# Performance work log

Hardware: AMD Instinct MI355X
Metric: run time of the kernel (lower is better)

The kernel has to match this reference:

```python
import jax, jax.numpy as jnp
import numpy as np

EPS = 1e-6

def poincare_pairwise_distance(x, c):
    """x: (B,N,E) points in Poincare ball, c: (C,E) centroids. Returns (B,N,C)."""
    x2 = jnp.sum(x * x, axis=-1)                  # (B,N)
    c2 = jnp.sum(c * c, axis=-1)                  # (C,)
    xc = jnp.einsum('bne,ce->bnc', x, c)          # (B,N,C)
    sq = jnp.maximum(x2[..., None] + c2[None, None, :] - 2.0 * xc, 0.0)  # ||x-c||^2
    den = (1.0 - x2)[..., None] * (1.0 - c2)[None, None, :]
    arg = 1.0 + 2.0 * sq / jnp.maximum(den, EPS)
    return jnp.arccosh(jnp.maximum(arg, 1.0 + EPS))

def setup_inputs() -> dict:
    key = jax.random.key(0)
    k1, k2 = jax.random.split(key)
    B, N, E, C = 32, 4096, 64, 256
    # scale so points lie strictly inside the unit ball (valid hyperbolic coords)
    node_repr = jax.random.normal(k1, (B, N, E), dtype=jnp.float32) * 0.05
    mask = jnp.ones((B, N, 1), dtype=jnp.float32)
    centroid = jax.random.normal(k2, (C, E), dtype=jnp.float32) * 0.01
    return {"node_repr": node_repr, "mask": mask, "centroid": centroid}

def reference(node_repr, mask, centroid):
    dist = poincare_pairwise_distance(node_repr, centroid)   # (B,N,C)
    dist = dist * mask                                       # mask: (B,N,1) broadcasts
    graph_dist = jnp.sum(dist, axis=1) / jnp.sum(mask, axis=1)  # (B,C)
    return graph_dist, dist
```

## Files before the change

### kernel.cpp

```cpp
#include <hip/hip_runtime.h>
#include <math.h>

#define E_DIM 64
#define C_DIM 256
#define EPS_F 1e-6f
#define LN2_F 0.69314718056f
#define TP    68

typedef __attribute__((ext_vector_type(8))) short short8;
typedef __attribute__((ext_vector_type(4))) float f32x4;

__device__ __forceinline__ unsigned short f2bf(float f) {
    unsigned int u = __float_as_uint(f);
    u += 0x7FFFu + ((u >> 16) & 1u);
    return (unsigned short)(u >> 16);
}

__device__ __forceinline__ short8 pack8(float4 a, float4 b) {
    short8 h;
    h[0] = (short)f2bf(a.x); h[1] = (short)f2bf(a.y);
    h[2] = (short)f2bf(a.z); h[3] = (short)f2bf(a.w);
    h[4] = (short)f2bf(b.x); h[5] = (short)f2bf(b.y);
    h[6] = (short)f2bf(b.z); h[7] = (short)f2bf(b.w);
    return h;
}

#define WS_F    0
#define WS_C2   32768
#define WS_RD2  33792
#define WS_INVM 34816

__global__ __launch_bounds__(C_DIM) void cdist_pre(
    const float* __restrict__ cent,
    const float* __restrict__ mask,
    unsigned char* __restrict__ ws,
    int N)
{
    const int t = threadIdx.x;
    if (blockIdx.x == 0) {
        float r[E_DIM];
        const float* cr = cent + t * E_DIM;
        #pragma unroll
        for (int e = 0; e < E_DIM; e += 4) {
            float4 v = *reinterpret_cast<const float4*>(cr + e);
            r[e] = v.x; r[e+1] = v.y; r[e+2] = v.z; r[e+3] = v.w;
        }
        float c2 = 0.f;
        #pragma unroll
        for (int e = 0; e < E_DIM; ++e) c2 = fmaf(r[e], r[e], c2);
        ((float*)(ws + WS_C2))[t]  = c2;
        ((float*)(ws + WS_RD2))[t] = 2.f / (1.f - c2);

        const int ct16 = t >> 4, l15 = t & 15;
        short8* F = (short8*)(ws + WS_F);
        #pragma unroll
        for (int kf = 0; kf < 2; ++kf) {
            #pragma unroll
            for (int q = 0; q < 4; ++q) {
                short8 h;
                #pragma unroll
                for (int j = 0; j < 8; ++j)
                    h[j] = (short)f2bf(r[kf * 32 + q * 8 + j]);
                F[(ct16 * 2 + kf) * 64 + 16 * q + l15] = h;
            }
        }
    } else {
        const int b = blockIdx.x - 1;
        float s = 0.f;
        for (int n = t; n < N; n += C_DIM) s += mask[(size_t)b * N + n];
        #pragma unroll
        for (int off = 32; off > 0; off >>= 1) s += __shfl_down(s, off, 64);
        __shared__ float partial[4];
        if ((t & 63) == 0) partial[t >> 6] = s;
        __syncthreads();
        if (t == 0) {
            float tot = partial[0] + partial[1] + partial[2] + partial[3];
            ((float*)(ws + WS_INVM))[b] = 1.f / tot;
        }
    }
}

template<int NT_TILES>
__global__ __launch_bounds__(256, 4) void cdist_mfma(
    const float* __restrict__ x,
    const float* __restrict__ mask,
    const unsigned char* __restrict__ ws,
    float*       __restrict__ graph_acc,
    float*       __restrict__ dist,
    int N)
{
    const int tid  = threadIdx.x;
    const int w    = tid >> 6;
    const int lane = tid & 63;
    const int l15  = lane & 15;
    const int q    = lane >> 4;
    const int n0   = blockIdx.x * (NT_TILES * 16);
    const int b    = blockIdx.y;

    __shared__ __align__(16) float sT[4][16 * TP];

    const short8* F    = (const short8*)(ws + WS_F);
    const float*  c2w  = (const float*)(ws + WS_C2);
    const float*  rd2w = (const float*)(ws + WS_RD2);

    short8 bfrag[4][2];
    #pragma unroll
    for (int ct = 0; ct < 4; ++ct)
        #pragma unroll
        for (int kf = 0; kf < 2; ++kf)
            bfrag[ct][kf] = F[((w * 4 + ct) * 2 + kf) * 64 + lane];

    float c2v[4], rd2v[4], gsum[4];
    #pragma unroll
    for (int ct = 0; ct < 4; ++ct) {
        const int c = w * 64 + ct * 16 + l15;
        c2v[ct] = c2w[c]; rd2v[ct] = rd2w[c]; gsum[ct] = 0.f;
    }

    const size_t rowbase = (size_t)b * N + n0;
    float* sW = sT[w];

    const float* xr0 = x + (rowbase + l15) * E_DIM + q * 8;
    float4 v0 = *reinterpret_cast<const float4*>(xr0);
    float4 v1 = *reinterpret_cast<const float4*>(xr0 + 4);
    float4 v2 = *reinterpret_cast<const float4*>(xr0 + 32);
    float4 v3 = *reinterpret_cast<const float4*>(xr0 + 36);
    float  mk = mask[rowbase + l15];

    #pragma unroll 1
    for (int rt = 0; rt < NT_TILES; ++rt) {
        float4 u0 = v0, u1 = v1, u2 = v2, u3 = v3;
        float  mkc = mk;

        if (rt < NT_TILES - 1) {
            const float* xr = x + (rowbase + (rt + 1) * 16 + l15) * E_DIM + q * 8;
            v0 = *reinterpret_cast<const float4*>(xr);
            v1 = *reinterpret_cast<const float4*>(xr + 4);
            v2 = *reinterpret_cast<const float4*>(xr + 32);
            v3 = *reinterpret_cast<const float4*>(xr + 36);
            mk = mask[rowbase + (rt + 1) * 16 + l15];
        }

        float ss = 0.f;
        ss = fmaf(u0.x, u0.x, ss); ss = fmaf(u0.y, u0.y, ss);
        ss = fmaf(u0.z, u0.z, ss); ss = fmaf(u0.w, u0.w, ss);
        ss = fmaf(u1.x, u1.x, ss); ss = fmaf(u1.y, u1.y, ss);
        ss = fmaf(u1.z, u1.z, ss); ss = fmaf(u1.w, u1.w, ss);
        ss = fmaf(u2.x, u2.x, ss); ss = fmaf(u2.y, u2.y, ss);
        ss = fmaf(u2.z, u2.z, ss); ss = fmaf(u2.w, u2.w, ss);
        ss = fmaf(u3.x, u3.x, ss); ss = fmaf(u3.y, u3.y, ss);
        ss = fmaf(u3.z, u3.z, ss); ss = fmaf(u3.w, u3.w, ss);
        ss += __shfl_xor(ss, 16);
        ss += __shfl_xor(ss, 32);

        const float rbrow = __builtin_amdgcn_rcpf(1.f - ss);
        const float krow  = LN2_F * mkc;

        short8 a0 = pack8(u0, u1);
        short8 a1 = pack8(u2, u3);

        f32x4 acc[4];
        #pragma unroll
        for (int ct = 0; ct < 4; ++ct) {
            f32x4 z = {0.f, 0.f, 0.f, 0.f};
            z = __builtin_amdgcn_mfma_f32_16x16x32_bf16(a0, bfrag[ct][0], z, 0, 0, 0);
            z = __builtin_amdgcn_mfma_f32_16x16x32_bf16(a1, bfrag[ct][1], z, 0, 0, 0);
            acc[ct] = z;
        }

        float ar[4], rbr[4], kr[4];
        #pragma unroll
        for (int reg = 0; reg < 4; ++reg) {
            const int src = q * 4 + reg;
            ar[reg]  = __shfl(ss,    src);
            rbr[reg] = __shfl(rbrow, src);
            kr[reg]  = __shfl(krow,  src);
        }

        #pragma unroll
        for (int ct = 0; ct < 4; ++ct) {
            #pragma unroll
            for (int reg = 0; reg < 4; ++reg) {
                const float dot = acc[ct][reg];
                float sq = fmaf(-2.f, dot, ar[reg] + c2v[ct]);
                sq = fmaxf(sq, 0.f);
                float uu = fmaxf(sq * (rbr[reg] * rd2v[ct]), EPS_F);
                float t  = uu + __builtin_amdgcn_sqrtf(fmaf(uu, uu, uu + uu));
                const float d = __builtin_amdgcn_logf(1.f + t) * kr[reg];
                sW[(q * 4 + reg) * TP + ct * 16 + l15] = d;
                gsum[ct] += d;
            }
        }

        #pragma unroll
        for (int i = 0; i < 4; ++i) {
            const int row2 = i * 4 + (lane >> 4);
            const int col2 = (lane & 15) * 4;
            f32x4 val = *reinterpret_cast<const f32x4*>(&sW[row2 * TP + col2]);
            __builtin_nontemporal_store(val, reinterpret_cast<f32x4*>(
                dist + (rowbase + rt * 16 + row2) * C_DIM + w * 64 + col2));
        }
    }

    const float inv = ((const float*)(ws + WS_INVM))[b];
    #pragma unroll
    for (int ct = 0; ct < 4; ++ct) {
        float s = gsum[ct];
        s += __shfl_xor(s, 16);
        s += __shfl_xor(s, 32);
        if (q == 0)
            atomicAdd(&graph_acc[b * C_DIM + w * 64 + ct * 16 + l15], s * inv);
    }
}

extern "C" void kernel_launch(void* const* d_in, const int* in_sizes, int n_in,
                              void* d_out, int out_size, void* d_ws, size_t ws_size,
                              hipStream_t stream) {
    const float* x    = (const float*)d_in[0];
    const float* mask = (const float*)d_in[1];
    const float* cent = (const float*)d_in[2];
    float* out = (float*)d_out;

    const long long BN = in_sizes[1];
    const int E = in_sizes[0] / (int)BN;
    const int C = in_sizes[2] / E;
    const int B = (int)(((long long)out_size - BN * C) / C);
    const int N = (int)(BN / B);

    float* graph_acc = out;
    float* dist_out  = out + (size_t)B * C;
    unsigned char* ws = (unsigned char*)d_ws;

    hipMemsetAsync(graph_acc, 0, (size_t)B * C * sizeof(float), stream);

    cdist_pre<<<dim3(B + 1), C_DIM, 0, stream>>>(cent, mask, ws, N);

    if (N % 128 == 0) {
        cdist_mfma<8><<<dim3(N / 128, B), 256, 0, stream>>>(
            x, mask, ws, graph_acc, dist_out, N);
    } else {
        cdist_mfma<4><<<dim3(N / 64, B), 256, 0, stream>>>(
            x, mask, ws, graph_acc, dist_out, N);
    }
}
```

Measured before the change: 184.4 us.

## Deepen x prefetch to two tiles and fold graph_acc zeroing into pre-kernel

The input prefetch in the main MFMA kernel now holds two tiles in a double-buffered register array and issues each load two iterations ahead, with the loop unrolled by two. This gives global loads more time to land before they are consumed. Separately, the hipMemsetAsync launch is removed and the mask-sum blocks of the pre-kernel zero graph_acc instead, saving one launch. The deeper prefetch raises register pressure, which may hurt occupancy under the 4-waves launch bound.

```diff
diff --git a/kernel.cpp b/kernel.cpp
--- a/kernel.cpp
+++ b/kernel.cpp
@@ -34,6 +34,7 @@
     const float* __restrict__ cent,
     const float* __restrict__ mask,
     unsigned char* __restrict__ ws,
+    float* __restrict__ graph_acc,
     int N)
 {
     const int t = threadIdx.x;
@@ -66,6 +67,7 @@
         }
     } else {
         const int b = blockIdx.x - 1;
+        graph_acc[b * C_DIM + t] = 0.f;
         float s = 0.f;
         for (int n = t; n < N; n += C_DIM) s += mask[(size_t)b * N + n];
         #pragma unroll
@@ -120,26 +122,28 @@
     const size_t rowbase = (size_t)b * N + n0;
     float* sW = sT[w];
 
-    const float* xr0 = x + (rowbase + l15) * E_DIM + q * 8;
-    float4 v0 = *reinterpret_cast<const float4*>(xr0);
-    float4 v1 = *reinterpret_cast<const float4*>(xr0 + 4);
-    float4 v2 = *reinterpret_cast<const float4*>(xr0 + 32);
-    float4 v3 = *reinterpret_cast<const float4*>(xr0 + 36);
-    float  mk = mask[rowbase + l15];
-
-    #pragma unroll 1
+    float4 pv0[2], pv1[2], pv2[2], pv3[2];
+    float  pmk[2];
+    {
+        const float* xr0 = x + (rowbase + l15) * E_DIM + q * 8;
+        pv0[0] = *reinterpret_cast<const float4*>(xr0);
+        pv1[0] = *reinterpret_cast<const float4*>(xr0 + 4);
+        pv2[0] = *reinterpret_cast<const float4*>(xr0 + 32);
+        pv3[0] = *reinterpret_cast<const float4*>(xr0 + 36);
+        pmk[0] = mask[rowbase + l15];
+        const float* xr1 = xr0 + 16 * E_DIM;
+        pv0[1] = *reinterpret_cast<const float4*>(xr1);
+        pv1[1] = *reinterpret_cast<const float4*>(xr1 + 4);
+        pv2[1] = *reinterpret_cast<const float4*>(xr1 + 32);
+        pv3[1] = *reinterpret_cast<const float4*>(xr1 + 36);
+        pmk[1] = mask[rowbase + 16 + l15];
+    }
+
+    #pragma unroll 2
     for (int rt = 0; rt < NT_TILES; ++rt) {
-        float4 u0 = v0, u1 = v1, u2 = v2, u3 = v3;
-        float  mkc = mk;
-
-        if (rt < NT_TILES - 1) {
-            const float* xr = x + (rowbase + (rt + 1) * 16 + l15) * E_DIM + q * 8;
-            v0 = *reinterpret_cast<const float4*>(xr);
-            v1 = *reinterpret_cast<const float4*>(xr + 4);
-            v2 = *reinterpret_cast<const float4*>(xr + 32);
-            v3 = *reinterpret_cast<const float4*>(xr + 36);
-            mk = mask[rowbase + (rt + 1) * 16 + l15];
-        }
+        const int s = rt & 1;
+        const float4 u0 = pv0[s], u1 = pv1[s], u2 = pv2[s], u3 = pv3[s];
+        const float  mkc = pmk[s];
 
         float ss = 0.f;
         ss = fmaf(u0.x, u0.x, ss); ss = fmaf(u0.y, u0.y, ss);
@@ -158,6 +162,15 @@
 
         short8 a0 = pack8(u0, u1);
         short8 a1 = pack8(u2, u3);
+
+        if (rt + 2 < NT_TILES) {
+            const float* xr = x + (rowbase + (rt + 2) * 16 + l15) * E_DIM + q * 8;
+            pv0[s] = *reinterpret_cast<const float4*>(xr);
+            pv1[s] = *reinterpret_cast<const float4*>(xr + 4);
+            pv2[s] = *reinterpret_cast<const float4*>(xr + 32);
+            pv3[s] = *reinterpret_cast<const float4*>(xr + 36);
+            pmk[s] = mask[rowbase + (rt + 2) * 16 + l15];
+        }
 
         f32x4 acc[4];
         #pragma unroll
@@ -231,9 +244,7 @@
     float* dist_out  = out + (size_t)B * C;
     unsigned char* ws = (unsigned char*)d_ws;
 
-    hipMemsetAsync(graph_acc, 0, (size_t)B * C * sizeof(float), stream);
-
-    cdist_pre<<<dim3(B + 1), C_DIM, 0, stream>>>(cent, mask, ws, N);
+    cdist_pre<<<dim3(B + 1), C_DIM, 0, stream>>>(cent, mask, ws, graph_acc, N);
 
     if (N % 128 == 0) {
         cdist_mfma<8><<<dim3(N / 128, B), 256, 0, stream>>>(
```

Measured after the change: 214.0 us. +16.1%, slower.

## Swap MFMA operands to write dist directly, drop LDS transpose and memset

Applied to the files above, without the earlier changes.

Swaps the A/B operands of the MFMA so each lane holds four consecutive centroid columns of one row. Each lane can then write a 16-byte vector straight to global memory, which removes the shared-memory transpose and the row-statistic shuffles. It also zeroes graph_acc inside the pre-kernel instead of a separate memset, splits the squared-norm reduction into four independent chains, and always uses 4-tile blocks. In exchange, the stores become normal rather than nontemporal with a 256-byte stride per lane group, the reduction needs more shuffles, and the grid doubles with more atomics.

```diff
diff --git a/kernel.cpp b/kernel.cpp
--- a/kernel.cpp
+++ b/kernel.cpp
@@ -5,7 +5,6 @@
 #define C_DIM 256
 #define EPS_F 1e-6f
 #define LN2_F 0.69314718056f
-#define TP    68
 
 typedef __attribute__((ext_vector_type(8))) short short8;
 typedef __attribute__((ext_vector_type(4))) float f32x4;
@@ -34,6 +33,7 @@
     const float* __restrict__ cent,
     const float* __restrict__ mask,
     unsigned char* __restrict__ ws,
+    float* __restrict__ graph_acc,
     int N)
 {
     const int t = threadIdx.x;
@@ -66,6 +66,7 @@
         }
     } else {
         const int b = blockIdx.x - 1;
+        graph_acc[b * C_DIM + t] = 0.f;
         float s = 0.f;
         for (int n = t; n < N; n += C_DIM) s += mask[(size_t)b * N + n];
         #pragma unroll
@@ -97,8 +98,6 @@
     const int n0   = blockIdx.x * (NT_TILES * 16);
     const int b    = blockIdx.y;
 
-    __shared__ __align__(16) float sT[4][16 * TP];
-
     const short8* F    = (const short8*)(ws + WS_F);
     const float*  c2w  = (const float*)(ws + WS_C2);
     const float*  rd2w = (const float*)(ws + WS_RD2);
@@ -110,15 +109,16 @@
         for (int kf = 0; kf < 2; ++kf)
             bfrag[ct][kf] = F[((w * 4 + ct) * 2 + kf) * 64 + lane];
 
-    float c2v[4], rd2v[4], gsum[4];
+    f32x4 c2q[4], rd2q[4], gsum[4];
     #pragma unroll
     for (int ct = 0; ct < 4; ++ct) {
-        const int c = w * 64 + ct * 16 + l15;
-        c2v[ct] = c2w[c]; rd2v[ct] = rd2w[c]; gsum[ct] = 0.f;
+        const int c = w * 64 + ct * 16 + q * 4;
+        c2q[ct]  = *reinterpret_cast<const f32x4*>(c2w + c);
+        rd2q[ct] = *reinterpret_cast<const f32x4*>(rd2w + c);
+        gsum[ct] = (f32x4){0.f, 0.f, 0.f, 0.f};
     }
 
     const size_t rowbase = (size_t)b * N + n0;
-    float* sW = sT[w];
 
     const float* xr0 = x + (rowbase + l15) * E_DIM + q * 8;
     float4 v0 = *reinterpret_cast<const float4*>(xr0);
@@ -129,10 +129,10 @@
 
     #pragma unroll 1
     for (int rt = 0; rt < NT_TILES; ++rt) {
-        float4 u0 = v0, u1 = v1, u2 = v2, u3 = v3;
-        float  mkc = mk;
-
-        if (rt < NT_TILES - 1) {
+        const float4 u0 = v0, u1 = v1, u2 = v2, u3 = v3;
+        const float  mkc = mk;
+
+        if (rt + 1 < NT_TILES) {
             const float* xr = x + (rowbase + (rt + 1) * 16 + l15) * E_DIM + q * 8;
             v0 = *reinterpret_cast<const float4*>(xr);
             v1 = *reinterpret_cast<const float4*>(xr + 4);
@@ -141,75 +141,62 @@
             mk = mask[rowbase + (rt + 1) * 16 + l15];
         }
 
-        float ss = 0.f;
-        ss = fmaf(u0.x, u0.x, ss); ss = fmaf(u0.y, u0.y, ss);
-        ss = fmaf(u0.z, u0.z, ss); ss = fmaf(u0.w, u0.w, ss);
-        ss = fmaf(u1.x, u1.x, ss); ss = fmaf(u1.y, u1.y, ss);
-        ss = fmaf(u1.z, u1.z, ss); ss = fmaf(u1.w, u1.w, ss);
-        ss = fmaf(u2.x, u2.x, ss); ss = fmaf(u2.y, u2.y, ss);
-        ss = fmaf(u2.z, u2.z, ss); ss = fmaf(u2.w, u2.w, ss);
-        ss = fmaf(u3.x, u3.x, ss); ss = fmaf(u3.y, u3.y, ss);
-        ss = fmaf(u3.z, u3.z, ss); ss = fmaf(u3.w, u3.w, ss);
+        float sa = 0.f, sb = 0.f, sc = 0.f, sd = 0.f;
+        sa = fmaf(u0.x, u0.x, sa); sa = fmaf(u0.y, u0.y, sa);
+        sa = fmaf(u0.z, u0.z, sa); sa = fmaf(u0.w, u0.w, sa);
+        sb = fmaf(u1.x, u1.x, sb); sb = fmaf(u1.y, u1.y, sb);
+        sb = fmaf(u1.z, u1.z, sb); sb = fmaf(u1.w, u1.w, sb);
+        sc = fmaf(u2.x, u2.x, sc); sc = fmaf(u2.y, u2.y, sc);
+        sc = fmaf(u2.z, u2.z, sc); sc = fmaf(u2.w, u2.w, sc);
+        sd = fmaf(u3.x, u3.x, sd); sd = fmaf(u3.y, u3.y, sd);
+        sd = fmaf(u3.z, u3.z, sd); sd = fmaf(u3.w, u3.w, sd);
+        float ss = (sa + sb) + (sc + sd);
         ss += __shfl_xor(ss, 16);
         ss += __shfl_xor(ss, 32);
 
         const float rbrow = __builtin_amdgcn_rcpf(1.f - ss);
         const float krow  = LN2_F * mkc;
 
-        short8 a0 = pack8(u0, u1);
-        short8 a1 = pack8(u2, u3);
-
-        f32x4 acc[4];
+        const short8 a0 = pack8(u0, u1);
+        const short8 a1 = pack8(u2, u3);
+
+        float* drow = dist + (rowbase + rt * 16 + l15) * C_DIM + w * 64;
+
         #pragma unroll
         for (int ct = 0; ct < 4; ++ct) {
             f32x4 z = {0.f, 0.f, 0.f, 0.f};
-            z = __builtin_amdgcn_mfma_f32_16x16x32_bf16(a0, bfrag[ct][0], z, 0, 0, 0);
-            z = __builtin_amdgcn_mfma_f32_16x16x32_bf16(a1, bfrag[ct][1], z, 0, 0, 0);
-            acc[ct] = z;
-        }
-
-        float ar[4], rbr[4], kr[4];
-        #pragma unroll
-        for (int reg = 0; reg < 4; ++reg) {
-            const int src = q * 4 + reg;
-            ar[reg]  = __shfl(ss,    src);
-            rbr[reg] = __shfl(rbrow, src);
-            kr[reg]  = __shfl(krow,  src);
-        }
-
-        #pragma unroll
-        for (int ct = 0; ct < 4; ++ct) {
+            z = __builtin_amdgcn_mfma_f32_16x16x32_bf16(bfrag[ct][0], a0, z, 0, 0, 0);
+            z = __builtin_amdgcn_mfma_f32_16x16x32_bf16(bfrag[ct][1], a1, z, 0, 0, 0);
+
+            f32x4 dv;
             #pragma unroll
             for (int reg = 0; reg < 4; ++reg) {
-                const float dot = acc[ct][reg];
-                float sq = fmaf(-2.f, dot, ar[reg] + c2v[ct]);
+                float sq = fmaf(-2.f, z[reg], ss + c2q[ct][reg]);
                 sq = fmaxf(sq, 0.f);
-                float uu = fmaxf(sq * (rbr[reg] * rd2v[ct]), EPS_F);
+                float uu = fmaxf(sq * (rbrow * rd2q[ct][reg]), EPS_F);
                 float t  = uu + __builtin_amdgcn_sqrtf(fmaf(uu, uu, uu + uu));
-                const float d = __builtin_amdgcn_logf(1.f + t) * kr[reg];
-                sW[(q * 4 + reg) * TP + ct * 16 + l15] = d;
-                gsum[ct] += d;
+                const float d = __builtin_amdgcn_logf(1.f + t) * krow;
+                dv[reg] = d;
+                gsum[ct][reg] += d;
             }
-        }
-
-        #pragma unroll
-        for (int i = 0; i < 4; ++i) {
-            const int row2 = i * 4 + (lane >> 4);
-            const int col2 = (lane & 15) * 4;
-            f32x4 val = *reinterpret_cast<const f32x4*>(&sW[row2 * TP + col2]);
-            __builtin_nontemporal_store(val, reinterpret_cast<f32x4*>(
-                dist + (rowbase + rt * 16 + row2) * C_DIM + w * 64 + col2));
+            *reinterpret_cast<f32x4*>(drow + ct * 16 + q * 4) = dv;
         }
     }
 
     const float inv = ((const float*)(ws + WS_INVM))[b];
     #pragma unroll
     for (int ct = 0; ct < 4; ++ct) {
-        float s = gsum[ct];
-        s += __shfl_xor(s, 16);
-        s += __shfl_xor(s, 32);
-        if (q == 0)
-            atomicAdd(&graph_acc[b * C_DIM + w * 64 + ct * 16 + l15], s * inv);
+        #pragma unroll
+        for (int reg = 0; reg < 4; ++reg) {
+            float s = gsum[ct][reg];
+            s += __shfl_xor(s, 1);
+            s += __shfl_xor(s, 2);
+            s += __shfl_xor(s, 4);
+            s += __shfl_xor(s, 8);
+            if (l15 == 0)
+                atomicAdd(&graph_acc[b * C_DIM + w * 64 + ct * 16 + q * 4 + reg],
+                          s * inv);
+        }
     }
 }
 
@@ -231,15 +218,8 @@
     float* dist_out  = out + (size_t)B * C;
     unsigned char* ws = (unsigned char*)d_ws;
 
-    hipMemsetAsync(graph_acc, 0, (size_t)B * C * sizeof(float), stream);
-
-    cdist_pre<<<dim3(B + 1), C_DIM, 0, stream>>>(cent, mask, ws, N);
-
-    if (N % 128 == 0) {
-        cdist_mfma<8><<<dim3(N / 128, B), 256, 0, stream>>>(
-            x, mask, ws, graph_acc, dist_out, N);
-    } else {
-        cdist_mfma<4><<<dim3(N / 64, B), 256, 0, stream>>>(
-            x, mask, ws, graph_acc, dist_out, N);
-    }
-}
+    cdist_pre<<<dim3(B + 1), C_DIM, 0, stream>>>(cent, mask, ws, graph_acc, N);
+
+    cdist_mfma<4><<<dim3(N / 64, B), 256, 0, stream>>>(
+        x, mask, ws, graph_acc, dist_out, N);
+}
```

Result: slower. 203.4 us (+10.3%).
